# Kernel optimization log

Hardware: AMD Instinct MI355X
Metric: run time of the kernel (lower is better)

The kernel has to match this reference:

```python
import jax, jax.numpy as jnp
import numpy as np

B, T, D = 2, 1024, 1024
V = 50257
K = 20  # n_noise_samples


def setup_inputs() -> dict:
    key = jax.random.key(0)
    k1, k2, k3, k4 = jax.random.split(key, 4)
    hidden = jax.random.normal(k1, (B, T, D), dtype=jnp.float32)
    targets = jax.random.randint(k2, (B, T), 0, V, dtype=jnp.int32)
    W = jax.random.normal(k3, (V, D), dtype=jnp.float32) * 0.02  # output_proj weight (V, D)
    noise_ids = jax.random.randint(k4, (K,), 0, V, dtype=jnp.int32)
    return {"hidden": hidden, "targets": targets, "W": W, "noise_ids": noise_ids}


def reference(hidden, targets, W, noise_ids):
    b, t, d = hidden.shape
    n = b * t
    h = hidden.reshape(n, d)            # (N, D)
    tgt = targets.reshape(n)            # (N,)
    # full-vocab projection, as in nn.Linear(d_model, vocab, bias=False)
    logits = h @ W.T                    # (N, V); temperature == 1.0 -> no-op
    scores_pos = logits[jnp.arange(n), tgt]                 # (N,)
    scores_neg = logits[:, noise_ids].reshape(-1)           # (N*K,)
    k = noise_ids.shape[0]
    log_k = jnp.log(jnp.float32(k))
    log_unif = -jnp.log(jnp.float32(W.shape[0]))            # sampler is None -> uniform noise
    pos_terms = jax.nn.log_sigmoid(scores_pos - log_k - log_unif)
    neg_terms = jax.nn.log_sigmoid(-(scores_neg - log_k - log_unif))
    loss = -pos_terms.mean() - neg_terms.mean()
    return loss
```

## Files before the change

### kernel.cpp

```cpp
#include <hip/hip_runtime.h>
#include <cmath>


#define KN 20

__device__ __forceinline__ float log_sigmoid_f(float x) {
    return fminf(x, 0.0f) - log1pf(expf(-fabsf(x)));
}

__device__ __forceinline__ float fma4(float4 a, float4 b, float acc) {
    acc = fmaf(a.x, b.x, acc);
    acc = fmaf(a.y, b.y, acc);
    acc = fmaf(a.z, b.z, acc);
    return fmaf(a.w, b.w, acc);
}

__device__ __forceinline__ float wave_reduce(float v) {
    #pragma unroll
    for (int off = 32; off > 0; off >>= 1) v += __shfl_xor(v, off, 64);
    return v;
}

__global__ __launch_bounds__(512) void nce_rows2_kernel(
    const float* __restrict__ hidden,
    const int*   __restrict__ targets,
    const float* __restrict__ W,
    const int*   __restrict__ noise_ids,
    float* __restrict__ cbw,
    float inv_n, float inv_nk, float shift)
{
    __shared__ float hlds[2048];

    const int tid  = threadIdx.x;
    const int wave = tid >> 6;
    const int lane = tid & 63;
    const int r0   = blockIdx.x * 2;

    reinterpret_cast<float4*>(hlds)[tid] =
        reinterpret_cast<const float4*>(hidden + (size_t)r0 * 1024)[tid];

    const int tgt0 = targets[r0];
    const int tgt1 = targets[r0 + 1];
    __syncthreads();

    float acc[3][2];
    #pragma unroll
    for (int s = 0; s < 3; ++s) { acc[s][0] = 0.0f; acc[s][1] = 0.0f; }

    #pragma unroll
    for (int s = 0; s < 2; ++s) {
        const int n = wave + 8 * s;
        const float* wr = W + (size_t)noise_ids[n] * 1024;
        #pragma unroll
        for (int j = 0; j < 4; ++j) {
            const float4 b  = *reinterpret_cast<const float4*>(wr + lane * 4 + j * 256);
            const float4 a0 = *reinterpret_cast<const float4*>(hlds + lane * 4 + j * 256);
            const float4 a1 = *reinterpret_cast<const float4*>(hlds + 1024 + lane * 4 + j * 256);
            acc[s][0] = fma4(b, a0, acc[s][0]);
            acc[s][1] = fma4(b, a1, acc[s][1]);
        }
    }

    if (wave < 4) {
        const float* wr = W + (size_t)noise_ids[16 + wave] * 1024;
        #pragma unroll
        for (int j = 0; j < 4; ++j) {
            const float4 b  = *reinterpret_cast<const float4*>(wr + lane * 4 + j * 256);
            const float4 a0 = *reinterpret_cast<const float4*>(hlds + lane * 4 + j * 256);
            const float4 a1 = *reinterpret_cast<const float4*>(hlds + 1024 + lane * 4 + j * 256);
            acc[2][0] = fma4(b, a0, acc[2][0]);
            acc[2][1] = fma4(b, a1, acc[2][1]);
        }
    } else if (wave < 6) {
        const int r = wave - 4;
        const float* wr = W + (size_t)(r == 0 ? tgt0 : tgt1) * 1024;
        const float* hr = hlds + r * 1024;
        #pragma unroll
        for (int j = 0; j < 4; ++j) {
            const float4 b = *reinterpret_cast<const float4*>(wr + lane * 4 + j * 256);
            const float4 a = *reinterpret_cast<const float4*>(hr + lane * 4 + j * 256);
            acc[2][0] = fma4(b, a, acc[2][0]);
        }
    }

    #pragma unroll
    for (int off = 32; off > 0; off >>= 1)
        #pragma unroll
        for (int s = 0; s < 3; ++s) {
            acc[s][0] += __shfl_xor(acc[s][0], off, 64);
            acc[s][1] += __shfl_xor(acc[s][1], off, 64);
        }

    float v = acc[0][0];
    v = (lane == 1) ? acc[0][1] : v;
    v = (lane == 2) ? acc[1][0] : v;
    v = (lane == 3) ? acc[1][1] : v;
    v = (lane == 4) ? acc[2][0] : v;
    v = (lane == 5) ? acc[2][1] : v;

    float term = 0.0f;
    if (lane < 6) {
        const bool valid  = (lane < 4) || (wave < 4) || (lane == 4 && wave < 6);
        const bool is_pos = (lane == 4 && wave >= 4);
        if (valid) {
            const float sc = v + shift;
            term = is_pos ? (-log_sigmoid_f(sc)) * inv_n
                          : (-log_sigmoid_f(-sc)) * inv_nk;
        }
    }
    term += __shfl_xor(term, 1, 64);
    term += __shfl_xor(term, 2, 64);
    term += __shfl_xor(term, 4, 64);

    if (lane == 0) cbw[blockIdx.x * 8 + wave] = term;
}

__global__ __launch_bounds__(256) void nce_generic_kernel(
    const float* __restrict__ hidden, const int* __restrict__ targets,
    const float* __restrict__ W, const int* __restrict__ noise_ids,
    float* __restrict__ cb4, int D, int K, float inv_n, float inv_nk, float shift)
{
    const int row  = blockIdx.x;
    const int tid  = threadIdx.x;
    const int wave = tid >> 6;
    const int lane = tid & 63;

    const float* hrow = hidden + (size_t)row * D;
    const int tgt = targets[row];
    float c = 0.0f;
    for (int id = wave; id <= K; id += 4) {
        const int wrow = (id == 0) ? tgt : noise_ids[id - 1];
        const float* wv = W + (size_t)wrow * D;
        float acc = 0.0f;
        for (int k = lane; k < D; k += 64) acc = fmaf(hrow[k], wv[k], acc);
        acc = wave_reduce(acc);
        if (lane == 0) {
            const float s = acc + shift;
            c += (id == 0) ? (-log_sigmoid_f(s)) * inv_n
                           : (-log_sigmoid_f(-s)) * inv_nk;
        }
    }
    if (lane == 0) cb4[row * 4 + wave] = c;
}

__global__ __launch_bounds__(256) void nce_sum_kernel(
    const float* __restrict__ cbw, float* __restrict__ out, int n4)
{
    __shared__ float sp[4];
    const int tid  = threadIdx.x;
    const int wave = tid >> 6;
    const int lane = tid & 63;

    const float4* v = reinterpret_cast<const float4*>(cbw);
    const int nv = n4 >> 2;
    float p = 0.0f;
    for (int i = tid; i < nv; i += 256) {
        const float4 x = v[i];
        p += (x.x + x.y) + (x.z + x.w);
    }
    p = wave_reduce(p);
    if (lane == 0) sp[wave] = p;
    __syncthreads();
    if (tid == 0) out[0] = sp[0] + sp[1] + sp[2] + sp[3];
}

extern "C" void kernel_launch(void* const* d_in, const int* in_sizes, int n_in,
                              void* d_out, int out_size, void* d_ws, size_t ws_size,
                              hipStream_t stream) {
    const float* hidden    = (const float*)d_in[0];
    const int*   targets   = (const int*)d_in[1];
    const float* W         = (const float*)d_in[2];
    const int*   noise_ids = (const int*)d_in[3];

    const int N = in_sizes[1];
    const int D = in_sizes[0] / N;
    const int K = in_sizes[3];
    const int V = in_sizes[2] / D;

    const float shift  = logf((float)V) - logf((float)K);
    const float inv_n  = 1.0f / (float)N;
    const float inv_nk = 1.0f / ((float)N * (float)K);

    float* cbw = (float*)d_ws;

    if (D == 1024 && K == KN && (N % 2) == 0) {
        nce_rows2_kernel<<<N / 2, 512, 0, stream>>>(
            hidden, targets, W, noise_ids, cbw, inv_n, inv_nk, shift);
    } else {
        nce_generic_kernel<<<N, 256, 0, stream>>>(
            hidden, targets, W, noise_ids, cbw, D, K, inv_n, inv_nk, shift);
    }
    nce_sum_kernel<<<1, 256, 0, stream>>>(cbw, (float*)d_out, 4 * N);
}
```

Measured before the change: 16.47 us.

## Process four rows per block with 1024 threads to reuse noise weight rows

Each block now handles four hidden rows with sixteen waves. Each wave loads one noise weight row into registers and dots it against all four rows. Waves 0-3 compute the target dot products, and waves 8-15 split the remaining four noise rows across row pairs. This halves the number of blocks and doubles the reuse of each noise weight row loaded from global/L2. The cost is larger blocks, more LDS per block, and some idle waves (4-7) in the second phase.

```diff
diff --git a/kernel.cpp b/kernel.cpp
--- a/kernel.cpp
+++ b/kernel.cpp
@@ -21,7 +21,7 @@
     return v;
 }
 
-__global__ __launch_bounds__(512) void nce_rows2_kernel(
+__global__ __launch_bounds__(1024) void nce_rows4_kernel(
     const float* __restrict__ hidden,
     const int*   __restrict__ targets,
     const float* __restrict__ W,
@@ -29,79 +29,85 @@
     float* __restrict__ cbw,
     float inv_n, float inv_nk, float shift)
 {
-    __shared__ float hlds[2048];
+    __shared__ float hlds[4096];
 
     const int tid  = threadIdx.x;
     const int wave = tid >> 6;
     const int lane = tid & 63;
-    const int r0   = blockIdx.x * 2;
+    const int r0   = blockIdx.x * 4;
 
     reinterpret_cast<float4*>(hlds)[tid] =
         reinterpret_cast<const float4*>(hidden + (size_t)r0 * 1024)[tid];
 
-    const int tgt0 = targets[r0];
-    const int tgt1 = targets[r0 + 1];
+    const int tgtw = targets[r0 + (wave & 3)];
     __syncthreads();
 
-    float acc[3][2];
-    #pragma unroll
-    for (int s = 0; s < 3; ++s) { acc[s][0] = 0.0f; acc[s][1] = 0.0f; }
-
-    #pragma unroll
-    for (int s = 0; s < 2; ++s) {
-        const int n = wave + 8 * s;
-        const float* wr = W + (size_t)noise_ids[n] * 1024;
+    const float* wr0 = W + (size_t)noise_ids[wave] * 1024;
+    float4 b0[4];
+    #pragma unroll
+    for (int j = 0; j < 4; ++j)
+        b0[j] = *reinterpret_cast<const float4*>(wr0 + lane * 4 + j * 256);
+
+    float a0[4] = {0.0f, 0.0f, 0.0f, 0.0f};
+    #pragma unroll
+    for (int r = 0; r < 4; ++r)
         #pragma unroll
         for (int j = 0; j < 4; ++j) {
-            const float4 b  = *reinterpret_cast<const float4*>(wr + lane * 4 + j * 256);
-            const float4 a0 = *reinterpret_cast<const float4*>(hlds + lane * 4 + j * 256);
-            const float4 a1 = *reinterpret_cast<const float4*>(hlds + 1024 + lane * 4 + j * 256);
-            acc[s][0] = fma4(b, a0, acc[s][0]);
-            acc[s][1] = fma4(b, a1, acc[s][1]);
-        }
-    }
-
+            const float4 hv = *reinterpret_cast<const float4*>(
+                hlds + r * 1024 + lane * 4 + j * 256);
+            a0[r] = fma4(b0[j], hv, a0[r]);
+        }
+
+    float accT = 0.0f, aP0 = 0.0f, aP1 = 0.0f;
     if (wave < 4) {
-        const float* wr = W + (size_t)noise_ids[16 + wave] * 1024;
-        #pragma unroll
-        for (int j = 0; j < 4; ++j) {
-            const float4 b  = *reinterpret_cast<const float4*>(wr + lane * 4 + j * 256);
-            const float4 a0 = *reinterpret_cast<const float4*>(hlds + lane * 4 + j * 256);
-            const float4 a1 = *reinterpret_cast<const float4*>(hlds + 1024 + lane * 4 + j * 256);
-            acc[2][0] = fma4(b, a0, acc[2][0]);
-            acc[2][1] = fma4(b, a1, acc[2][1]);
-        }
-    } else if (wave < 6) {
-        const int r = wave - 4;
-        const float* wr = W + (size_t)(r == 0 ? tgt0 : tgt1) * 1024;
-        const float* hr = hlds + r * 1024;
+        const float* wr = W + (size_t)tgtw * 1024;
+        const float* hr = hlds + wave * 1024;
         #pragma unroll
         for (int j = 0; j < 4; ++j) {
             const float4 b = *reinterpret_cast<const float4*>(wr + lane * 4 + j * 256);
             const float4 a = *reinterpret_cast<const float4*>(hr + lane * 4 + j * 256);
-            acc[2][0] = fma4(b, a, acc[2][0]);
-        }
-    }
-
-    #pragma unroll
-    for (int off = 32; off > 0; off >>= 1)
-        #pragma unroll
-        for (int s = 0; s < 3; ++s) {
-            acc[s][0] += __shfl_xor(acc[s][0], off, 64);
-            acc[s][1] += __shfl_xor(acc[s][1], off, 64);
-        }
-
-    float v = acc[0][0];
-    v = (lane == 1) ? acc[0][1] : v;
-    v = (lane == 2) ? acc[1][0] : v;
-    v = (lane == 3) ? acc[1][1] : v;
-    v = (lane == 4) ? acc[2][0] : v;
-    v = (lane == 5) ? acc[2][1] : v;
+            accT = fma4(b, a, accT);
+        }
+    } else if (wave >= 8) {
+        const int p  = wave - 8;
+        const int n1 = 16 + (p >> 1);
+        const int rb = 2 * (p & 1);
+        const float* wr = W + (size_t)noise_ids[n1] * 1024;
+        #pragma unroll
+        for (int j = 0; j < 4; ++j) {
+            const float4 b  = *reinterpret_cast<const float4*>(wr + lane * 4 + j * 256);
+            const float4 h0 = *reinterpret_cast<const float4*>(
+                hlds + rb * 1024 + lane * 4 + j * 256);
+            const float4 h1 = *reinterpret_cast<const float4*>(
+                hlds + (rb + 1) * 1024 + lane * 4 + j * 256);
+            aP0 = fma4(b, h0, aP0);
+            aP1 = fma4(b, h1, aP1);
+        }
+    }
+
+    #pragma unroll
+    for (int off = 32; off > 0; off >>= 1) {
+        #pragma unroll
+        for (int r = 0; r < 4; ++r) a0[r] += __shfl_xor(a0[r], off, 64);
+        accT += __shfl_xor(accT, off, 64);
+        aP0  += __shfl_xor(aP0,  off, 64);
+        aP1  += __shfl_xor(aP1,  off, 64);
+    }
+
+    float v = a0[0];
+    v = (lane == 1) ? a0[1] : v;
+    v = (lane == 2) ? a0[2] : v;
+    v = (lane == 3) ? a0[3] : v;
+    v = (lane == 4) ? accT  : v;
+    v = (lane == 5) ? aP0   : v;
+    v = (lane == 6) ? aP1   : v;
 
     float term = 0.0f;
-    if (lane < 6) {
-        const bool valid  = (lane < 4) || (wave < 4) || (lane == 4 && wave < 6);
-        const bool is_pos = (lane == 4 && wave >= 4);
+    {
+        const bool is_pos = (lane == 4);
+        const bool valid  = (lane < 4)
+                          | (lane == 4 && wave < 4)
+                          | ((lane == 5 || lane == 6) && wave >= 8);
         if (valid) {
             const float sc = v + shift;
             term = is_pos ? (-log_sigmoid_f(sc)) * inv_n
@@ -112,7 +118,7 @@
     term += __shfl_xor(term, 2, 64);
     term += __shfl_xor(term, 4, 64);
 
-    if (lane == 0) cbw[blockIdx.x * 8 + wave] = term;
+    if (lane == 0) cbw[blockIdx.x * 16 + wave] = term;
 }
 
 __global__ __launch_bounds__(256) void nce_generic_kernel(
@@ -183,8 +189,8 @@
 
     float* cbw = (float*)d_ws;
 
-    if (D == 1024 && K == KN && (N % 2) == 0) {
-        nce_rows2_kernel<<<N / 2, 512, 0, stream>>>(
+    if (D == 1024 && K == KN && (N % 4) == 0) {
+        nce_rows4_kernel<<<N / 4, 1024, 0, stream>>>(
             hidden, targets, W, noise_ids, cbw, inv_n, inv_nk, shift);
     } else {
         nce_generic_kernel<<<N, 256, 0, stream>>>(
```

Result: slower. 17.46 us (+6.0%).
